# Kernel tuning notes

Measured on AMD Instinct MI355X. Metric: run time of the kernel, lower is better.

## Reference

```python
import jax, jax.numpy as jnp
import numpy as np

B, L, D = 2, 2048, 1024
DH = 64
NH = D // DH
EPS = 1e-5
NEG = -1e30


def rms_norm(x, w):
    # x: (..., dh); norm in fp32 like the torch module, then scale by weight
    xf = x.astype(jnp.float32)
    y = xf * jax.lax.rsqrt(jnp.mean(xf * xf, axis=-1, keepdims=True) + EPS)
    return y.astype(x.dtype) * w.astype(x.dtype)


def sdpa(q, k, v, m):
    # q:(b,h,lq,dh) k,v:(b,h,lk,dh) m:(lq,lk) bool
    scale = 1.0 / jnp.sqrt(jnp.asarray(DH, q.dtype))
    s = jnp.einsum('bhqd,bhkd->bhqk', q, k) * scale
    s = jnp.where(m[None, None], s, NEG)
    p = jax.nn.softmax(s, axis=-1)
    return jnp.einsum('bhqk,bhkd->bhqd', p, v)


def setup_inputs() -> dict:
    key = jax.random.key(0)
    k1, k2, k3 = jax.random.split(key, 3)
    x = jax.random.normal(k1, (B, L, D), dtype=jnp.float32)
    mask = jnp.tril(jnp.ones((L, L), dtype=bool))  # causal: no fully-masked rows
    w_qkv = jax.random.normal(k2, (3 * D, D), dtype=jnp.float32) * (1.0 / np.sqrt(D))
    w_fc = jax.random.normal(k3, (D, D), dtype=jnp.float32) * (1.0 / np.sqrt(D))
    q_norm_w = jnp.ones((DH,), dtype=jnp.float32)
    k_norm_w = jnp.ones((DH,), dtype=jnp.float32)
    return {"x": x, "mask": mask, "w_qkv": w_qkv, "w_fc": w_fc,
            "q_norm_w": q_norm_w, "k_norm_w": k_norm_w,
            "subset_attention_size": 1024}


def reference(x, mask, w_qkv, w_fc, q_norm_w, k_norm_w, subset_attention_size):
    b, l, d = x.shape
    qkv = jnp.einsum('bld,ed->ble', x, w_qkv)  # (b,l,3d)
    q, k, v = jnp.split(qkv, 3, axis=-1)

    def heads(t):
        return t.reshape(b, l, NH, DH).transpose(0, 2, 1, 3)  # (b,nh,l,dh)

    q, k, v = heads(q), heads(k), heads(v)
    q = rms_norm(q, q_norm_w)
    k = rms_norm(k, k_norm_w)

    S = subset_attention_size
    if S is not None and S < l:
        o1 = sdpa(q[:, :, :S], k[:, :, :S], v[:, :, :S], mask[:S, :S])
        o2 = sdpa(q[:, :, S:], k, v, mask[S:, :])
        o = jnp.concatenate([o1, o2], axis=2)
    else:
        o = sdpa(q, k, v, mask)
    o = o.transpose(0, 2, 1, 3).reshape(b, l, d)  # (b,l,d)
    return jnp.einsum('bld,ed->ble', o, w_fc)
```

## Files before the change

### kernel.cpp

```cpp
#include <hip/hip_runtime.h>

typedef __bf16 bf16x8 __attribute__((ext_vector_type(8)));
typedef __bf16 bf16x4 __attribute__((ext_vector_type(4)));
typedef float f32x4 __attribute__((ext_vector_type(4)));
typedef unsigned short u16;
typedef unsigned int u32;
typedef unsigned short u16x4 __attribute__((ext_vector_type(4)));
typedef unsigned short u16x8 __attribute__((ext_vector_type(8)));

#define AS1 __attribute__((address_space(1)))
#define AS3 __attribute__((address_space(3)))

__device__ __forceinline__ u16 f2bf(float f) {
  unsigned u = __builtin_bit_cast(unsigned, f);
  u += 0x7fffu + ((u >> 16) & 1u);
  return (u16)(u >> 16);
}

__global__ __launch_bounds__(256) void cvt_all(const float* __restrict__ x,
                                               const float* __restrict__ wq,
                                               const float* __restrict__ wf,
                                               u16* __restrict__ xb, u16* __restrict__ wqb,
                                               u16* __restrict__ wfb) {
  long i = ((long)blockIdx.x * 256 + threadIdx.x) * 4;
  const float* src;
  u16* dst;
  long off;
  if (i < 4194304L) {
    src = x; dst = xb; off = i;
  } else if (i < 7340032L) {
    src = wq; dst = wqb; off = i - 4194304L;
  } else {
    src = wf; dst = wfb; off = i - 7340032L;
  }
  float4 v = *reinterpret_cast<const float4*>(src + off);
  u16x4 o;
  o.x = f2bf(v.x); o.y = f2bf(v.y); o.z = f2bf(v.z); o.w = f2bf(v.w);
  *reinterpret_cast<u16x4*>(dst + off) = o;
}

__global__ __launch_bounds__(256, 2) void gemm_qkv(const u16* __restrict__ A,
                                                   const u16* __restrict__ W,
                                                   u16* __restrict__ C,
                                                   const float* __restrict__ qw,
                                                   const float* __restrict__ kw) {
  constexpr int N = 3072, K = 1024;
  __shared__ __align__(16) u16 As[128 * 32];
  __shared__ __align__(16) u16 Bs[128 * 32];
  const int tid = threadIdx.x;
  const int lane = tid & 63;
  const int wid = tid >> 6;
  const int wm = wid >> 1, wn = wid & 1;
  const int l16 = lane & 15, g4 = lane >> 4;
  const long bm = blockIdx.x, bn = blockIdx.y;

  const int srow = tid >> 2;
  const int scol = (tid & 3) * 8;
  const u16* aA0 = A + (bm * 128 + srow) * (long)K + scol;
  const u16* aA1 = aA0 + 64 * (long)K;
  const u16* aW0 = W + (bn * 128 + srow) * (long)K + scol;
  const u16* aW1 = aW0 + 64 * (long)K;

  f32x4 acc[4][4] = {};

  for (int kt = 0; kt < K; kt += 32) {
    __builtin_amdgcn_global_load_lds((AS1 void*)(aA0 + kt), (AS3 void*)(&As[tid * 8]), 16, 0, 0);
    __builtin_amdgcn_global_load_lds((AS1 void*)(aA1 + kt), (AS3 void*)(&As[2048 + tid * 8]), 16, 0, 0);
    __builtin_amdgcn_global_load_lds((AS1 void*)(aW0 + kt), (AS3 void*)(&Bs[tid * 8]), 16, 0, 0);
    __builtin_amdgcn_global_load_lds((AS1 void*)(aW1 + kt), (AS3 void*)(&Bs[2048 + tid * 8]), 16, 0, 0);
    __syncthreads();
    bf16x8 af[4], bfr[4];
#pragma unroll
    for (int m = 0; m < 4; ++m)
      af[m] = *reinterpret_cast<const bf16x8*>(&As[(wm * 64 + m * 16 + l16) * 32 + g4 * 8]);
#pragma unroll
    for (int n = 0; n < 4; ++n)
      bfr[n] = *reinterpret_cast<const bf16x8*>(&Bs[(wn * 64 + n * 16 + l16) * 32 + g4 * 8]);
#pragma unroll
    for (int m = 0; m < 4; ++m)
#pragma unroll
      for (int n = 0; n < 4; ++n)
        acc[m][n] = __builtin_amdgcn_mfma_f32_16x16x32_bf16(af[m], bfr[n], acc[m][n], 0, 0, 0);
    __syncthreads();
  }

  if (bn < 16) {
    const float qscale = 0.18033688011112042f;
    const float* w = (bn < 8) ? qw : kw;
    const float ws = (bn < 8) ? qscale : 1.0f;
    float wv[4];
#pragma unroll
    for (int n = 0; n < 4; ++n) wv[n] = w[n * 16 + l16] * ws;
#pragma unroll
    for (int m = 0; m < 4; ++m) {
#pragma unroll
      for (int j = 0; j < 4; ++j) {
        float ss = 0.f;
#pragma unroll
        for (int n = 0; n < 4; ++n) ss = fmaf(acc[m][n][j], acc[m][n][j], ss);
        ss += __shfl_xor(ss, 1);
        ss += __shfl_xor(ss, 2);
        ss += __shfl_xor(ss, 4);
        ss += __shfl_xor(ss, 8);
        const float inv = rsqrtf(ss * (1.0f / 64.0f) + 1e-5f);
#pragma unroll
        for (int n = 0; n < 4; ++n) acc[m][n][j] *= inv * wv[n];
      }
    }
  }

#pragma unroll
  for (int m = 0; m < 4; ++m)
#pragma unroll
    for (int n = 0; n < 4; ++n)
#pragma unroll
      for (int j = 0; j < 4; ++j) {
        long row = bm * 128 + wm * 64 + m * 16 + g4 * 4 + j;
        long col = bn * 128 + wn * 64 + n * 16 + l16;
        C[row * N + col] = f2bf(acc[m][n][j]);
      }
}

__global__ __launch_bounds__(256, 2) void gemm_fc(const u16* __restrict__ A,
                                                  const u16* __restrict__ W,
                                                  float* __restrict__ C) {
  constexpr int N = 1024, K = 1024;
  __shared__ __align__(16) u16 As[128 * 32];
  __shared__ __align__(16) u16 Bs[64 * 32];
  const int tid = threadIdx.x;
  const int lane = tid & 63;
  const int wid = tid >> 6;
  const int wm = wid >> 1, wn = wid & 1;
  const int l16 = lane & 15, g4 = lane >> 4;
  const long bm = blockIdx.x, bn = blockIdx.y;

  const int srow = tid >> 2;
  const int scol = (tid & 3) * 8;
  const u16* aA0 = A + (bm * 128 + srow) * (long)K + scol;
  const u16* aA1 = aA0 + 64 * (long)K;
  const u16* aW0 = W + (bn * 64 + srow) * (long)K + scol;

  f32x4 acc[4][2] = {};

  for (int kt = 0; kt < K; kt += 32) {
    __builtin_amdgcn_global_load_lds((AS1 void*)(aA0 + kt), (AS3 void*)(&As[tid * 8]), 16, 0, 0);
    __builtin_amdgcn_global_load_lds((AS1 void*)(aA1 + kt), (AS3 void*)(&As[2048 + tid * 8]), 16, 0, 0);
    __builtin_amdgcn_global_load_lds((AS1 void*)(aW0 + kt), (AS3 void*)(&Bs[tid * 8]), 16, 0, 0);
    __syncthreads();
    bf16x8 af[4], bfr[2];
#pragma unroll
    for (int m = 0; m < 4; ++m)
      af[m] = *reinterpret_cast<const bf16x8*>(&As[(wm * 64 + m * 16 + l16) * 32 + g4 * 8]);
#pragma unroll
    for (int n = 0; n < 2; ++n)
      bfr[n] = *reinterpret_cast<const bf16x8*>(&Bs[(wn * 32 + n * 16 + l16) * 32 + g4 * 8]);
#pragma unroll
    for (int m = 0; m < 4; ++m)
#pragma unroll
      for (int n = 0; n < 2; ++n)
        acc[m][n] = __builtin_amdgcn_mfma_f32_16x16x32_bf16(af[m], bfr[n], acc[m][n], 0, 0, 0);
    __syncthreads();
  }

#pragma unroll
  for (int m = 0; m < 4; ++m)
#pragma unroll
    for (int n = 0; n < 2; ++n)
#pragma unroll
      for (int j = 0; j < 4; ++j) {
        long row = bm * 128 + wm * 64 + m * 16 + g4 * 4 + j;
        long col = bn * 64 + wn * 32 + n * 16 + l16;
        C[row * N + col] = acc[m][n][j];
      }
}

__global__ __launch_bounds__(256) void vtrans(const u16* __restrict__ qkv,
                                              u16* __restrict__ vt) {
  __shared__ u16 T[64][66];
  const int tid = threadIdx.x;
  const int f = blockIdx.x;
  const int bh = (f & 7) * 4 + (f >> 8);
  const int ktile = (f >> 3) & 31;
  const long vbase = (long)(bh >> 4) * 2048 * 3072 + (bh & 15) * 64 + 2048;
  const int r = tid >> 2, c = (tid & 3) * 16;
  const u16* src = qkv + vbase + (long)(ktile * 64 + r) * 3072 + c;
  *reinterpret_cast<u16x8*>(&T[r][c]) = *reinterpret_cast<const u16x8*>(src);
  *reinterpret_cast<u16x8*>(&T[r][c + 8]) = *reinterpret_cast<const u16x8*>(src + 8);
  __syncthreads();
  const int dr = tid >> 2, kc = (tid & 3) * 16;
  u16 buf[16];
#pragma unroll
  for (int j = 0; j < 16; ++j) buf[j] = T[kc + j][dr];
  u16* dst = vt + (long)bh * 131072 + (long)dr * 2048 + ktile * 64 + kc;
  *reinterpret_cast<u16x8*>(dst) = *reinterpret_cast<u16x8*>(&buf[0]);
  *reinterpret_cast<u16x8*>(dst + 8) = *reinterpret_cast<u16x8*>(&buf[8]);
}

__global__ __launch_bounds__(256, 4) void attn_causal(const u16* __restrict__ qkv,
                                                      const u16* __restrict__ vt,
                                                      u16* __restrict__ o) {
  __shared__ __align__(16) u16 Klds[2][4096];
  __shared__ __align__(16) u16 Vlds[2][4096];
  __shared__ __align__(16) u16 Plds[4][1024];

  const int tid = threadIdx.x, lane = tid & 63, wid = tid >> 6;
  const int l16 = lane & 15, g4 = lane >> 4;
  const int h8 = (l16 & 7) << 4;

  const int f = blockIdx.x;
  const int xcd = f & 7;
  const int g = f >> 3;
  const int hb = g >> 5;
  const int w = g & 31;
  const int bh = xcd * 4 + hb;
  const int basei = (w & 1) ? (31 - (w >> 1)) : (w >> 1);
  const int it = (hb & 1) ? (31 - basei) : basei;

  const long base = (long)(bh >> 4) * 2048 * 3072 + (bh & 15) * 64;
  const u16* qb = qkv + base;
  const u16* kb = qkv + base + 1024;
  const u16* vtb = vt + (long)bh * 131072;

  const u16* qp = qb + ((long)it * 64 + wid * 16 + l16) * 3072;
  const bf16x8 q0 = *reinterpret_cast<const bf16x8*>(qp + g4 * 8);
  const bf16x8 q1 = *reinterpret_cast<const bf16x8*>(qp + 32 + g4 * 8);

  f32x4 acc[4] = {};
  f32x4 lacc = {};

  bf16x8 ones;
#pragma unroll
  for (int j = 0; j < 8; ++j) ones[j] = (__bf16)1.0f;

  const int krow = tid >> 3;
  const int scolE = (((tid & 7) * 16) ^ ((krow & 7) << 4)) >> 1;

  auto stage_issue = [&](int buf, int kt) {
    __builtin_amdgcn_global_load_lds((AS1 void*)(kb + (long)(kt * 64 + krow) * 3072 + scolE),
                                     (AS3 void*)(&Klds[buf][tid * 8]), 16, 0, 0);
    __builtin_amdgcn_global_load_lds((AS1 void*)(kb + (long)(kt * 64 + krow + 32) * 3072 + scolE),
                                     (AS3 void*)(&Klds[buf][2048 + tid * 8]), 16, 0, 0);
    __builtin_amdgcn_global_load_lds((AS1 void*)(vtb + (long)krow * 2048 + kt * 64 + scolE),
                                     (AS3 void*)(&Vlds[buf][tid * 8]), 16, 0, 0);
    __builtin_amdgcn_global_load_lds((AS1 void*)(vtb + (long)(krow + 32) * 2048 + kt * 64 + scolE),
                                     (AS3 void*)(&Vlds[buf][2048 + tid * 8]), 16, 0, 0);
  };

  auto tile_step = [&](int cur, bool diag) {
    bf16x8 kf[4][2];
#pragma unroll
    for (int kn = 0; kn < 4; ++kn) {
      const int row = kn * 16 + l16;
#pragma unroll
      for (int ck = 0; ck < 2; ++ck)
        kf[kn][ck] = *reinterpret_cast<const bf16x8*>(
            &Klds[cur][row * 64 + (((ck * 64 + g4 * 16) ^ h8) >> 1)]);
    }
    f32x4 s[4];
    __builtin_amdgcn_s_setprio(1);
#pragma unroll
    for (int kn = 0; kn < 4; ++kn) {
      f32x4 z = {0.f, 0.f, 0.f, 0.f};
      z = __builtin_amdgcn_mfma_f32_16x16x32_bf16(kf[kn][0], q0, z, 0, 0, 0);
      z = __builtin_amdgcn_mfma_f32_16x16x32_bf16(kf[kn][1], q1, z, 0, 0, 0);
      s[kn] = z;
    }
    __builtin_amdgcn_s_setprio(0);
    if (diag) {
      const int qrel = wid * 16 + l16;
#pragma unroll
      for (int kn = 0; kn < 4; ++kn)
#pragma unroll
        for (int j = 0; j < 4; ++j)
          if (kn * 16 + g4 * 4 + j > qrel) s[kn][j] = -3e38f;
    }
#pragma unroll
    for (int kn = 0; kn < 4; ++kn)
#pragma unroll
      for (int j = 0; j < 4; ++j) s[kn][j] = exp2f(s[kn][j]);
    u16* pl = &Plds[wid][0];
#pragma unroll
    for (int kn = 0; kn < 4; ++kn) {
      bf16x4 w4;
      w4[0] = (__bf16)s[kn][0];
      w4[1] = (__bf16)s[kn][1];
      w4[2] = (__bf16)s[kn][2];
      w4[3] = (__bf16)s[kn][3];
      const int boff = (kn * 32 + g4 * 8) ^ h8;
      *reinterpret_cast<bf16x4*>(&pl[l16 * 64 + (boff >> 1)]) = w4;
    }
    const bf16x8 pa0 = *reinterpret_cast<const bf16x8*>(&pl[l16 * 64 + (((g4 * 16) ^ h8) >> 1)]);
    const bf16x8 pa1 =
        *reinterpret_cast<const bf16x8*>(&pl[l16 * 64 + (((64 + g4 * 16) ^ h8) >> 1)]);
    bf16x8 vf[4][2];
#pragma unroll
    for (int n = 0; n < 4; ++n) {
      const int row = n * 16 + l16;
#pragma unroll
      for (int ck = 0; ck < 2; ++ck)
        vf[n][ck] = *reinterpret_cast<const bf16x8*>(
            &Vlds[cur][row * 64 + (((ck * 64 + g4 * 16) ^ h8) >> 1)]);
    }
    __builtin_amdgcn_s_setprio(1);
    lacc = __builtin_amdgcn_mfma_f32_16x16x32_bf16(pa0, ones, lacc, 0, 0, 0);
    lacc = __builtin_amdgcn_mfma_f32_16x16x32_bf16(pa1, ones, lacc, 0, 0, 0);
#pragma unroll
    for (int n = 0; n < 4; ++n) {
      acc[n] = __builtin_amdgcn_mfma_f32_16x16x32_bf16(pa0, vf[n][0], acc[n], 0, 0, 0);
      acc[n] = __builtin_amdgcn_mfma_f32_16x16x32_bf16(pa1, vf[n][1], acc[n], 0, 0, 0);
    }
    __builtin_amdgcn_s_setprio(0);
  };

  stage_issue(0, 0);
  __syncthreads();

  for (int kt = 0; kt < it; ++kt) {
    const int cur = kt & 1;
    stage_issue(cur ^ 1, kt + 1);
    tile_step(cur, false);
    __syncthreads();
  }
  tile_step(it & 1, true);

  const long obase = (long)(bh >> 4) * 2048 * 1024 + (bh & 15) * 64;
  u16* op = o + obase + ((long)it * 64 + wid * 16 + g4 * 4) * 1024;
#pragma unroll
  for (int n = 0; n < 4; ++n)
#pragma unroll
    for (int j = 0; j < 4; ++j)
      op[j * 1024 + n * 16 + l16] = f2bf(acc[n][j] / lacc[j]);
}

extern "C" void kernel_launch(void* const* d_in, const int* in_sizes, int n_in,
                              void* d_out, int out_size, void* d_ws, size_t ws_size,
                              hipStream_t stream) {
  const float* x = (const float*)d_in[0];
  const float* w_qkv = (const float*)d_in[2];
  const float* w_fc = (const float*)d_in[3];
  const float* qw = (const float*)d_in[4];
  const float* kw = (const float*)d_in[5];
  float* out = (float*)d_out;

  char* ws = (char*)d_ws;
  u16* xb    = (u16*)(ws);
  u16* wqkvb = (u16*)(ws + (8L << 20));
  u16* wfcb  = (u16*)(ws + (14L << 20));
  u16* qkv   = (u16*)(ws + (16L << 20));
  u16* ob    = (u16*)(ws + (40L << 20));
  u16* vt    = xb;

  cvt_all<<<8192, 256, 0, stream>>>(x, w_qkv, w_fc, xb, wqkvb, wfcb);
  gemm_qkv<<<dim3(32, 24), 256, 0, stream>>>(xb, wqkvb, qkv, qw, kw);
  vtrans<<<1024, 256, 0, stream>>>(qkv, vt);
  attn_causal<<<1024, 256, 0, stream>>>(qkv, vt, ob);
  gemm_fc<<<dim3(32, 16), 256, 0, stream>>>(ob, wfcb, out);
}
```

Measured before the change: 111.4 us.

## Split attention key tile across waves and drop P LDS round-trip

The attention kernel now gives each wave 16 keys of every 64-key tile against all 64 queries, instead of 16 queries against all keys. The score accumulator layout feeds PV directly through 16x16x16 MFMAs, so the per-wave P buffer in LDS and the ones-vector row-sum MFMA go away. Q is staged in LDS, and row sums are accumulated in registers. The price is a cross-wave reduction at the end through LDS with several extra barriers, plus a 64-register accumulator per wave, which may lower occupancy under launch_bounds(256,4).

```diff
diff --git a/kernel.cpp b/kernel.cpp
--- a/kernel.cpp
+++ b/kernel.cpp
@@ -1,8 +1,8 @@
 #include <hip/hip_runtime.h>
 
 typedef __bf16 bf16x8 __attribute__((ext_vector_type(8)));
-typedef __bf16 bf16x4 __attribute__((ext_vector_type(4)));
 typedef float f32x4 __attribute__((ext_vector_type(4)));
+typedef short s16x4 __attribute__((ext_vector_type(4)));
 typedef unsigned short u16;
 typedef unsigned int u32;
 typedef unsigned short u16x4 __attribute__((ext_vector_type(4)));
@@ -15,6 +15,15 @@
   unsigned u = __builtin_bit_cast(unsigned, f);
   u += 0x7fffu + ((u >> 16) & 1u);
   return (u16)(u >> 16);
+}
+
+__device__ __forceinline__ f32x4 mfma16(s16x4 a, s16x4 b, f32x4 c) {
+#if __has_builtin(__builtin_amdgcn_mfma_f32_16x16x16bf16_1k)
+  return __builtin_amdgcn_mfma_f32_16x16x16bf16_1k(a, b, c, 0, 0, 0);
+#else
+  asm("v_mfma_f32_16x16x16_bf16 %0, %1, %2, %0" : "+v"(c) : "v"(a), "v"(b));
+  return c;
+#endif
 }
 
 __global__ __launch_bounds__(256) void cvt_all(const float* __restrict__ x,
@@ -201,7 +210,7 @@
                                                       u16* __restrict__ o) {
   __shared__ __align__(16) u16 Klds[2][4096];
   __shared__ __align__(16) u16 Vlds[2][4096];
-  __shared__ __align__(16) u16 Plds[4][1024];
+  __shared__ __align__(16) u16 Qlds[4096];
 
   const int tid = threadIdx.x, lane = tid & 63, wid = tid >> 6;
   const int l16 = lane & 15, g4 = lane >> 4;
@@ -221,19 +230,16 @@
   const u16* kb = qkv + base + 1024;
   const u16* vtb = vt + (long)bh * 131072;
 
-  const u16* qp = qb + ((long)it * 64 + wid * 16 + l16) * 3072;
-  const bf16x8 q0 = *reinterpret_cast<const bf16x8*>(qp + g4 * 8);
-  const bf16x8 q1 = *reinterpret_cast<const bf16x8*>(qp + 32 + g4 * 8);
-
-  f32x4 acc[4] = {};
-  f32x4 lacc = {};
-
-  bf16x8 ones;
-#pragma unroll
-  for (int j = 0; j < 8; ++j) ones[j] = (__bf16)1.0f;
+  f32x4 acc[4][4] = {};
+  float lp[4] = {};
 
   const int krow = tid >> 3;
   const int scolE = (((tid & 7) * 16) ^ ((krow & 7) << 4)) >> 1;
+
+  __builtin_amdgcn_global_load_lds((AS1 void*)(qb + (long)(it * 64 + krow) * 3072 + scolE),
+                                   (AS3 void*)(&Qlds[tid * 8]), 16, 0, 0);
+  __builtin_amdgcn_global_load_lds((AS1 void*)(qb + (long)(it * 64 + krow + 32) * 3072 + scolE),
+                                   (AS3 void*)(&Qlds[2048 + tid * 8]), 16, 0, 0);
 
   auto stage_issue = [&](int buf, int kt) {
     __builtin_amdgcn_global_load_lds((AS1 void*)(kb + (long)(kt * 64 + krow) * 3072 + scolE),
@@ -246,68 +252,60 @@
                                      (AS3 void*)(&Vlds[buf][2048 + tid * 8]), 16, 0, 0);
   };
 
+  const int vblk = ((((2 * wid + (g4 >> 1)) << 4) ^ h8) >> 1) + (g4 & 1) * 4;
+
   auto tile_step = [&](int cur, bool diag) {
-    bf16x8 kf[4][2];
-#pragma unroll
-    for (int kn = 0; kn < 4; ++kn) {
-      const int row = kn * 16 + l16;
-#pragma unroll
-      for (int ck = 0; ck < 2; ++ck)
-        kf[kn][ck] = *reinterpret_cast<const bf16x8*>(
-            &Klds[cur][row * 64 + (((ck * 64 + g4 * 16) ^ h8) >> 1)]);
-    }
+    const int krowL = wid * 16 + l16;
+    const bf16x8 kf0 = *reinterpret_cast<const bf16x8*>(
+        &Klds[cur][krowL * 64 + (((g4 * 16) ^ h8) >> 1)]);
+    const bf16x8 kf1 = *reinterpret_cast<const bf16x8*>(
+        &Klds[cur][krowL * 64 + (((64 + g4 * 16) ^ h8) >> 1)]);
     f32x4 s[4];
     __builtin_amdgcn_s_setprio(1);
 #pragma unroll
-    for (int kn = 0; kn < 4; ++kn) {
+    for (int qq = 0; qq < 4; ++qq) {
+      const int qrow = qq * 16 + l16;
+      const bf16x8 qf0 = *reinterpret_cast<const bf16x8*>(
+          &Qlds[qrow * 64 + (((g4 * 16) ^ h8) >> 1)]);
+      const bf16x8 qf1 = *reinterpret_cast<const bf16x8*>(
+          &Qlds[qrow * 64 + (((64 + g4 * 16) ^ h8) >> 1)]);
       f32x4 z = {0.f, 0.f, 0.f, 0.f};
-      z = __builtin_amdgcn_mfma_f32_16x16x32_bf16(kf[kn][0], q0, z, 0, 0, 0);
-      z = __builtin_amdgcn_mfma_f32_16x16x32_bf16(kf[kn][1], q1, z, 0, 0, 0);
-      s[kn] = z;
+      z = __builtin_amdgcn_mfma_f32_16x16x32_bf16(kf0, qf0, z, 0, 0, 0);
+      z = __builtin_amdgcn_mfma_f32_16x16x32_bf16(kf1, qf1, z, 0, 0, 0);
+      s[qq] = z;
     }
     __builtin_amdgcn_s_setprio(0);
     if (diag) {
-      const int qrel = wid * 16 + l16;
-#pragma unroll
-      for (int kn = 0; kn < 4; ++kn)
+      const int keyl = wid * 16 + g4 * 4;
+#pragma unroll
+      for (int qq = 0; qq < 4; ++qq) {
+        const int ql = qq * 16 + l16;
 #pragma unroll
         for (int j = 0; j < 4; ++j)
-          if (kn * 16 + g4 * 4 + j > qrel) s[kn][j] = -3e38f;
+          if (keyl + j > ql) s[qq][j] = -3e38f;
+      }
     }
-#pragma unroll
-    for (int kn = 0; kn < 4; ++kn)
-#pragma unroll
-      for (int j = 0; j < 4; ++j) s[kn][j] = exp2f(s[kn][j]);
-    u16* pl = &Plds[wid][0];
-#pragma unroll
-    for (int kn = 0; kn < 4; ++kn) {
-      bf16x4 w4;
-      w4[0] = (__bf16)s[kn][0];
-      w4[1] = (__bf16)s[kn][1];
-      w4[2] = (__bf16)s[kn][2];
-      w4[3] = (__bf16)s[kn][3];
-      const int boff = (kn * 32 + g4 * 8) ^ h8;
-      *reinterpret_cast<bf16x4*>(&pl[l16 * 64 + (boff >> 1)]) = w4;
-    }
-    const bf16x8 pa0 = *reinterpret_cast<const bf16x8*>(&pl[l16 * 64 + (((g4 * 16) ^ h8) >> 1)]);
-    const bf16x8 pa1 =
-        *reinterpret_cast<const bf16x8*>(&pl[l16 * 64 + (((64 + g4 * 16) ^ h8) >> 1)]);
-    bf16x8 vf[4][2];
-#pragma unroll
-    for (int n = 0; n < 4; ++n) {
-      const int row = n * 16 + l16;
-#pragma unroll
-      for (int ck = 0; ck < 2; ++ck)
-        vf[n][ck] = *reinterpret_cast<const bf16x8*>(
-            &Vlds[cur][row * 64 + (((ck * 64 + g4 * 16) ^ h8) >> 1)]);
+    s16x4 pfr[4];
+#pragma unroll
+    for (int qq = 0; qq < 4; ++qq) {
+#pragma unroll
+      for (int j = 0; j < 4; ++j) s[qq][j] = exp2f(s[qq][j]);
+      lp[qq] += s[qq][0] + s[qq][1] + s[qq][2] + s[qq][3];
+      s16x4 p;
+      p[0] = (short)f2bf(s[qq][0]);
+      p[1] = (short)f2bf(s[qq][1]);
+      p[2] = (short)f2bf(s[qq][2]);
+      p[3] = (short)f2bf(s[qq][3]);
+      pfr[qq] = p;
     }
     __builtin_amdgcn_s_setprio(1);
-    lacc = __builtin_amdgcn_mfma_f32_16x16x32_bf16(pa0, ones, lacc, 0, 0, 0);
-    lacc = __builtin_amdgcn_mfma_f32_16x16x32_bf16(pa1, ones, lacc, 0, 0, 0);
-#pragma unroll
-    for (int n = 0; n < 4; ++n) {
-      acc[n] = __builtin_amdgcn_mfma_f32_16x16x32_bf16(pa0, vf[n][0], acc[n], 0, 0, 0);
-      acc[n] = __builtin_amdgcn_mfma_f32_16x16x32_bf16(pa1, vf[n][1], acc[n], 0, 0, 0);
+#pragma unroll
+    for (int db = 0; db < 4; ++db) {
+      const int vrow = db * 16 + l16;
+      const u16x4 vv = *reinterpret_cast<const u16x4*>(&Vlds[cur][vrow * 64 + vblk]);
+      const s16x4 vf = __builtin_bit_cast(s16x4, vv);
+#pragma unroll
+      for (int qq = 0; qq < 4; ++qq) acc[qq][db] = mfma16(pfr[qq], vf, acc[qq][db]);
     }
     __builtin_amdgcn_s_setprio(0);
   };
@@ -322,14 +320,98 @@
     __syncthreads();
   }
   tile_step(it & 1, true);
-
+  __syncthreads();
+
+  float* red0 = reinterpret_cast<float*>(&Klds[0][0]);
+  float* red1 = reinterpret_cast<float*>(&Vlds[0][0]);
+  float* lsml = reinterpret_cast<float*>(&Qlds[0]);
+  float* lfin = lsml + 1024;
+
+#define OIDX(qq, db, j) ((qq * 16 + g4 * 4 + j) * 64 + db * 16 + l16)
+  if (wid == 2) {
+#pragma unroll
+    for (int qq = 0; qq < 4; ++qq)
+#pragma unroll
+      for (int db = 0; db < 4; ++db)
+#pragma unroll
+        for (int j = 0; j < 4; ++j) red0[OIDX(qq, db, j)] = acc[qq][db][j];
+  }
+  if (wid == 3) {
+#pragma unroll
+    for (int qq = 0; qq < 4; ++qq)
+#pragma unroll
+      for (int db = 0; db < 4; ++db)
+#pragma unroll
+        for (int j = 0; j < 4; ++j) red1[OIDX(qq, db, j)] = acc[qq][db][j];
+  }
+#pragma unroll
+  for (int qq = 0; qq < 4; ++qq) lsml[(qq * 16 + l16) * 16 + wid * 4 + g4] = lp[qq];
+  __syncthreads();
+  if (wid == 0) {
+#pragma unroll
+    for (int qq = 0; qq < 4; ++qq)
+#pragma unroll
+      for (int db = 0; db < 4; ++db)
+#pragma unroll
+        for (int j = 0; j < 4; ++j) acc[qq][db][j] += red0[OIDX(qq, db, j)];
+  }
+  if (wid == 1) {
+#pragma unroll
+    for (int qq = 0; qq < 4; ++qq)
+#pragma unroll
+      for (int db = 0; db < 4; ++db)
+#pragma unroll
+        for (int j = 0; j < 4; ++j) acc[qq][db][j] += red1[OIDX(qq, db, j)];
+  }
+  if (wid == 2) {
+    const float* b = &lsml[lane * 16];
+    f32x4 t0 = *reinterpret_cast<const f32x4*>(b);
+    f32x4 t1 = *reinterpret_cast<const f32x4*>(b + 4);
+    f32x4 t2 = *reinterpret_cast<const f32x4*>(b + 8);
+    f32x4 t3 = *reinterpret_cast<const f32x4*>(b + 12);
+    f32x4 t = t0 + t1 + t2 + t3;
+    lfin[lane] = t[0] + t[1] + t[2] + t[3];
+  }
+  __syncthreads();
+  if (wid == 1) {
+#pragma unroll
+    for (int qq = 0; qq < 4; ++qq)
+#pragma unroll
+      for (int db = 0; db < 4; ++db)
+#pragma unroll
+        for (int j = 0; j < 4; ++j) red0[OIDX(qq, db, j)] = acc[qq][db][j];
+  }
+  __syncthreads();
+  if (wid == 0) {
+#pragma unroll
+    for (int qq = 0; qq < 4; ++qq)
+#pragma unroll
+      for (int db = 0; db < 4; ++db)
+#pragma unroll
+        for (int j = 0; j < 4; ++j) red0[OIDX(qq, db, j)] += acc[qq][db][j];
+  }
+  __syncthreads();
+#undef OIDX
+
+  const int row = wid * 16 + l16;
+  const float linv = 1.0f / lfin[row];
+  const float* rr = &red0[row * 64 + g4 * 16];
+  f32x4 v0 = *reinterpret_cast<const f32x4*>(rr);
+  f32x4 v1 = *reinterpret_cast<const f32x4*>(rr + 4);
+  f32x4 v2 = *reinterpret_cast<const f32x4*>(rr + 8);
+  f32x4 v3 = *reinterpret_cast<const f32x4*>(rr + 12);
+  u16x8 oa, ob2;
+#pragma unroll
+  for (int j = 0; j < 4; ++j) {
+    oa[j] = f2bf(v0[j] * linv);
+    oa[j + 4] = f2bf(v1[j] * linv);
+    ob2[j] = f2bf(v2[j] * linv);
+    ob2[j + 4] = f2bf(v3[j] * linv);
+  }
   const long obase = (long)(bh >> 4) * 2048 * 1024 + (bh & 15) * 64;
-  u16* op = o + obase + ((long)it * 64 + wid * 16 + g4 * 4) * 1024;
-#pragma unroll
-  for (int n = 0; n < 4; ++n)
-#pragma unroll
-    for (int j = 0; j < 4; ++j)
-      op[j * 1024 + n * 16 + l16] = f2bf(acc[n][j] / lacc[j]);
+  u16* op = o + obase + (long)(it * 64 + row) * 1024 + g4 * 16;
+  *reinterpret_cast<u16x8*>(op) = oa;
+  *reinterpret_cast<u16x8*>(op + 8) = ob2;
 }
 
 extern "C" void kernel_launch(void* const* d_in, const int* in_sizes, int n_in,
```

Result: slower. 118.1 us (+6.0%).

## Split attention tile 2x2 across waves, keep P in registers via 16x16x16 MFMA

Applied to the files above, without the earlier changes.

Changes the per-block work split from four waves each owning 16 query rows to a 2x2 arrangement where each wave handles 32 queries and half of the keys. Probabilities now feed the PV matmul directly from registers using the 16x16x16 bf16 MFMA layout, which removes the P round-trip through LDS. The two key-halves are reduced through shared memory in the epilogue. The diagonal tile skips the wave whose quarter is fully masked. The trade-off is an extra LDS reduction and two more syncs at the end, a larger accumulator footprint, and use of the smaller-K MFMA instruction.

```diff
diff --git a/kernel.cpp b/kernel.cpp
--- a/kernel.cpp
+++ b/kernel.cpp
@@ -3,6 +3,7 @@
 typedef __bf16 bf16x8 __attribute__((ext_vector_type(8)));
 typedef __bf16 bf16x4 __attribute__((ext_vector_type(4)));
 typedef float f32x4 __attribute__((ext_vector_type(4)));
+typedef short s16x4 __attribute__((ext_vector_type(4)));
 typedef unsigned short u16;
 typedef unsigned int u32;
 typedef unsigned short u16x4 __attribute__((ext_vector_type(4)));
@@ -15,6 +16,15 @@
   unsigned u = __builtin_bit_cast(unsigned, f);
   u += 0x7fffu + ((u >> 16) & 1u);
   return (u16)(u >> 16);
+}
+
+__device__ __forceinline__ f32x4 mfma16(s16x4 a, s16x4 b, f32x4 c) {
+#if __has_builtin(__builtin_amdgcn_mfma_f32_16x16x16bf16_1k)
+  return __builtin_amdgcn_mfma_f32_16x16x16bf16_1k(a, b, c, 0, 0, 0);
+#else
+  asm("v_mfma_f32_16x16x16_bf16 %0, %1, %2, %0" : "+v"(c) : "v"(a), "v"(b));
+  return c;
+#endif
 }
 
 __global__ __launch_bounds__(256) void cvt_all(const float* __restrict__ x,
@@ -199,13 +209,12 @@
 __global__ __launch_bounds__(256, 4) void attn_causal(const u16* __restrict__ qkv,
                                                       const u16* __restrict__ vt,
                                                       u16* __restrict__ o) {
-  __shared__ __align__(16) u16 Klds[2][4096];
-  __shared__ __align__(16) u16 Vlds[2][4096];
-  __shared__ __align__(16) u16 Plds[4][1024];
+  __shared__ __align__(16) u16 SMEM[16384];
 
   const int tid = threadIdx.x, lane = tid & 63, wid = tid >> 6;
   const int l16 = lane & 15, g4 = lane >> 4;
   const int h8 = (l16 & 7) << 4;
+  const int qh = wid & 1, kh = wid >> 1;
 
   const int f = blockIdx.x;
   const int xcd = f & 7;
@@ -221,93 +230,101 @@
   const u16* kb = qkv + base + 1024;
   const u16* vtb = vt + (long)bh * 131072;
 
-  const u16* qp = qb + ((long)it * 64 + wid * 16 + l16) * 3072;
-  const bf16x8 q0 = *reinterpret_cast<const bf16x8*>(qp + g4 * 8);
-  const bf16x8 q1 = *reinterpret_cast<const bf16x8*>(qp + 32 + g4 * 8);
-
-  f32x4 acc[4] = {};
-  f32x4 lacc = {};
-
-  bf16x8 ones;
-#pragma unroll
-  for (int j = 0; j < 8; ++j) ones[j] = (__bf16)1.0f;
+  bf16x8 qv[2][2];
+#pragma unroll
+  for (int qf = 0; qf < 2; ++qf) {
+    const u16* qp = qb + ((long)it * 64 + qh * 32 + qf * 16 + l16) * 3072;
+    qv[qf][0] = *reinterpret_cast<const bf16x8*>(qp + g4 * 8);
+    qv[qf][1] = *reinterpret_cast<const bf16x8*>(qp + 32 + g4 * 8);
+  }
+
+  f32x4 acc[2][4] = {};
+  f32x4 lacc[2] = {};
+
+  s16x4 ones4;
+#pragma unroll
+  for (int j = 0; j < 4; ++j) ones4[j] = (short)0x3F80;
 
   const int krow = tid >> 3;
   const int scolE = (((tid & 7) * 16) ^ ((krow & 7) << 4)) >> 1;
 
   auto stage_issue = [&](int buf, int kt) {
+    u16* KB = SMEM + buf * 4096;
+    u16* VB = SMEM + 8192 + buf * 4096;
     __builtin_amdgcn_global_load_lds((AS1 void*)(kb + (long)(kt * 64 + krow) * 3072 + scolE),
-                                     (AS3 void*)(&Klds[buf][tid * 8]), 16, 0, 0);
+                                     (AS3 void*)(&KB[tid * 8]), 16, 0, 0);
     __builtin_amdgcn_global_load_lds((AS1 void*)(kb + (long)(kt * 64 + krow + 32) * 3072 + scolE),
-                                     (AS3 void*)(&Klds[buf][2048 + tid * 8]), 16, 0, 0);
+                                     (AS3 void*)(&KB[2048 + tid * 8]), 16, 0, 0);
     __builtin_amdgcn_global_load_lds((AS1 void*)(vtb + (long)krow * 2048 + kt * 64 + scolE),
-                                     (AS3 void*)(&Vlds[buf][tid * 8]), 16, 0, 0);
+                                     (AS3 void*)(&VB[tid * 8]), 16, 0, 0);
     __builtin_amdgcn_global_load_lds((AS1 void*)(vtb + (long)(krow + 32) * 2048 + kt * 64 + scolE),
-                                     (AS3 void*)(&Vlds[buf][2048 + tid * 8]), 16, 0, 0);
+                                     (AS3 void*)(&VB[2048 + tid * 8]), 16, 0, 0);
   };
 
   auto tile_step = [&](int cur, bool diag) {
-    bf16x8 kf[4][2];
-#pragma unroll
-    for (int kn = 0; kn < 4; ++kn) {
-      const int row = kn * 16 + l16;
+    if (diag && qh == 0 && kh == 1) return;
+    const u16* KB = SMEM + cur * 4096;
+    const u16* VB = SMEM + 8192 + cur * 4096;
+    bf16x8 kfr[2][2];
+#pragma unroll
+    for (int kf = 0; kf < 2; ++kf) {
+      const int row = kh * 32 + kf * 16 + l16;
 #pragma unroll
       for (int ck = 0; ck < 2; ++ck)
-        kf[kn][ck] = *reinterpret_cast<const bf16x8*>(
-            &Klds[cur][row * 64 + (((ck * 64 + g4 * 16) ^ h8) >> 1)]);
-    }
-    f32x4 s[4];
+        kfr[kf][ck] = *reinterpret_cast<const bf16x8*>(
+            &KB[row * 64 + (((ck * 64 + g4 * 16) ^ h8) >> 1)]);
+    }
+    f32x4 s[2][2];
     __builtin_amdgcn_s_setprio(1);
 #pragma unroll
-    for (int kn = 0; kn < 4; ++kn) {
-      f32x4 z = {0.f, 0.f, 0.f, 0.f};
-      z = __builtin_amdgcn_mfma_f32_16x16x32_bf16(kf[kn][0], q0, z, 0, 0, 0);
-      z = __builtin_amdgcn_mfma_f32_16x16x32_bf16(kf[kn][1], q1, z, 0, 0, 0);
-      s[kn] = z;
-    }
+    for (int kf = 0; kf < 2; ++kf)
+#pragma unroll
+      for (int qf = 0; qf < 2; ++qf) {
+        f32x4 z = {0.f, 0.f, 0.f, 0.f};
+        z = __builtin_amdgcn_mfma_f32_16x16x32_bf16(kfr[kf][0], qv[qf][0], z, 0, 0, 0);
+        z = __builtin_amdgcn_mfma_f32_16x16x32_bf16(kfr[kf][1], qv[qf][1], z, 0, 0, 0);
+        s[kf][qf] = z;
+      }
     __builtin_amdgcn_s_setprio(0);
     if (diag) {
-      const int qrel = wid * 16 + l16;
-#pragma unroll
-      for (int kn = 0; kn < 4; ++kn)
-#pragma unroll
-        for (int j = 0; j < 4; ++j)
-          if (kn * 16 + g4 * 4 + j > qrel) s[kn][j] = -3e38f;
-    }
-#pragma unroll
-    for (int kn = 0; kn < 4; ++kn)
-#pragma unroll
-      for (int j = 0; j < 4; ++j) s[kn][j] = exp2f(s[kn][j]);
-    u16* pl = &Plds[wid][0];
-#pragma unroll
-    for (int kn = 0; kn < 4; ++kn) {
-      bf16x4 w4;
-      w4[0] = (__bf16)s[kn][0];
-      w4[1] = (__bf16)s[kn][1];
-      w4[2] = (__bf16)s[kn][2];
-      w4[3] = (__bf16)s[kn][3];
-      const int boff = (kn * 32 + g4 * 8) ^ h8;
-      *reinterpret_cast<bf16x4*>(&pl[l16 * 64 + (boff >> 1)]) = w4;
-    }
-    const bf16x8 pa0 = *reinterpret_cast<const bf16x8*>(&pl[l16 * 64 + (((g4 * 16) ^ h8) >> 1)]);
-    const bf16x8 pa1 =
-        *reinterpret_cast<const bf16x8*>(&pl[l16 * 64 + (((64 + g4 * 16) ^ h8) >> 1)]);
-    bf16x8 vf[4][2];
-#pragma unroll
-    for (int n = 0; n < 4; ++n) {
-      const int row = n * 16 + l16;
-#pragma unroll
-      for (int ck = 0; ck < 2; ++ck)
-        vf[n][ck] = *reinterpret_cast<const bf16x8*>(
-            &Vlds[cur][row * 64 + (((ck * 64 + g4 * 16) ^ h8) >> 1)]);
-    }
+#pragma unroll
+      for (int kf = 0; kf < 2; ++kf)
+#pragma unroll
+        for (int qf = 0; qf < 2; ++qf) {
+          const int keyl = kh * 32 + kf * 16 + g4 * 4;
+          const int ql = qh * 32 + qf * 16 + l16;
+#pragma unroll
+          for (int j = 0; j < 4; ++j)
+            if (keyl + j > ql) s[kf][qf][j] = -3e38f;
+        }
+    }
+    s16x4 pfr[2][2];
+#pragma unroll
+    for (int kf = 0; kf < 2; ++kf)
+#pragma unroll
+      for (int qf = 0; qf < 2; ++qf) {
+        bf16x4 p;
+#pragma unroll
+        for (int j = 0; j < 4; ++j) p[j] = (__bf16)exp2f(s[kf][qf][j]);
+        pfr[kf][qf] = __builtin_bit_cast(s16x4, p);
+      }
     __builtin_amdgcn_s_setprio(1);
-    lacc = __builtin_amdgcn_mfma_f32_16x16x32_bf16(pa0, ones, lacc, 0, 0, 0);
-    lacc = __builtin_amdgcn_mfma_f32_16x16x32_bf16(pa1, ones, lacc, 0, 0, 0);
-#pragma unroll
-    for (int n = 0; n < 4; ++n) {
-      acc[n] = __builtin_amdgcn_mfma_f32_16x16x32_bf16(pa0, vf[n][0], acc[n], 0, 0, 0);
-      acc[n] = __builtin_amdgcn_mfma_f32_16x16x32_bf16(pa1, vf[n][1], acc[n], 0, 0, 0);
+#pragma unroll
+    for (int qf = 0; qf < 2; ++qf) {
+      lacc[qf] = mfma16(pfr[0][qf], ones4, lacc[qf]);
+      lacc[qf] = mfma16(pfr[1][qf], ones4, lacc[qf]);
+    }
+#pragma unroll
+    for (int db = 0; db < 4; ++db) {
+      const int vrow = db * 16 + l16;
+#pragma unroll
+      for (int kf = 0; kf < 2; ++kf) {
+        const u16x4 vv = *reinterpret_cast<const u16x4*>(
+            &VB[vrow * 64 + (((kh * 64 + kf * 32 + g4 * 8) ^ h8) >> 1)]);
+        const s16x4 vf = __builtin_bit_cast(s16x4, vv);
+#pragma unroll
+        for (int qf = 0; qf < 2; ++qf) acc[qf][db] = mfma16(pfr[kf][qf], vf, acc[qf][db]);
+      }
     }
     __builtin_amdgcn_s_setprio(0);
   };
@@ -322,14 +339,47 @@
     __syncthreads();
   }
   tile_step(it & 1, true);
-
-  const long obase = (long)(bh >> 4) * 2048 * 1024 + (bh & 15) * 64;
-  u16* op = o + obase + ((long)it * 64 + wid * 16 + g4 * 4) * 1024;
-#pragma unroll
-  for (int n = 0; n < 4; ++n)
-#pragma unroll
-    for (int j = 0; j < 4; ++j)
-      op[j * 1024 + n * 16 + l16] = f2bf(acc[n][j] / lacc[j]);
+  __syncthreads();
+
+  float* Ebuf = reinterpret_cast<float*>(SMEM);
+  const int ebase = qh * 2176;
+  if (kh == 1) {
+#pragma unroll
+    for (int qf = 0; qf < 2; ++qf) {
+#pragma unroll
+      for (int db = 0; db < 4; ++db)
+#pragma unroll
+        for (int j = 0; j < 4; ++j)
+          Ebuf[ebase + (qf * 16 + g4 * 4 + j) * 68 + db * 16 + l16] = acc[qf][db][j];
+      if (l16 == 0) {
+#pragma unroll
+        for (int j = 0; j < 4; ++j)
+          Ebuf[ebase + (qf * 16 + g4 * 4 + j) * 68 + 64] = lacc[qf][j];
+      }
+    }
+  }
+  __syncthreads();
+  if (kh == 0) {
+    const long obase = (long)(bh >> 4) * 2048 * 1024 + (bh & 15) * 64;
+#pragma unroll
+    for (int qf = 0; qf < 2; ++qf) {
+      float linv[4];
+#pragma unroll
+      for (int j = 0; j < 4; ++j) {
+        const float lsum = lacc[qf][j] + Ebuf[ebase + (qf * 16 + g4 * 4 + j) * 68 + 64];
+        linv[j] = 1.0f / lsum;
+      }
+#pragma unroll
+      for (int db = 0; db < 4; ++db)
+#pragma unroll
+        for (int j = 0; j < 4; ++j) {
+          const int row = qh * 32 + qf * 16 + g4 * 4 + j;
+          const float v =
+              acc[qf][db][j] + Ebuf[ebase + (qf * 16 + g4 * 4 + j) * 68 + db * 16 + l16];
+          o[obase + ((long)it * 64 + row) * 1024 + db * 16 + l16] = f2bf(v * linv[j]);
+        }
+    }
+  }
 }
 
 extern "C" void kernel_launch(void* const* d_in, const int* in_sizes, int n_in,
```

Measured after the change: 108.9 us. -2.2%, faster.
